# Optimization experiments

Hardware: AMD Instinct MI355X
Metric: run time of the kernel (lower is better)

The kernel has to match this reference:

```python
import jax, jax.numpy as jnp
import numpy as np

C, K, D, N = 8, 64, 32, 2048  # components, flow layers, obs dim, grid nodes


def setup_inputs() -> dict:
    key = jax.random.key(0)
    ks = jax.random.split(key, 16)
    def rn(k, shape, s=0.02):
        return (s * jax.random.normal(k, shape, dtype=jnp.float32))
    return {
        "nodes": jax.random.normal(ks[0], (N, D), dtype=jnp.float32),
        # coupling nets: MLP([D, 2D, D]) per layer per component (torch Linear layout: W [out,in])
        "s_W1": rn(ks[1], (C, K, 2 * D, D)), "s_b1": rn(ks[2], (C, K, 2 * D)),
        "s_W2": rn(ks[3], (C, K, D, 2 * D)), "s_b2": rn(ks[4], (C, K, D)),
        "t_W1": rn(ks[5], (C, K, 2 * D, D)), "t_b1": rn(ks[6], (C, K, 2 * D)),
        "t_W2": rn(ks[7], (C, K, D, 2 * D)), "t_b2": rn(ks[8], (C, K, D)),
        # ActNorm scale/shift per layer per component
        "an_s": rn(ks[9], (C, K, D), 0.01), "an_t": rn(ks[10], (C, K, D), 0.01),
        # DiagGaussian base distribution params per component
        "loc": rn(ks[11], (C, D), 0.1), "log_scale": rn(ks[12], (C, D), 0.1),
        # unconstrained joint S matrix
        "S_unc": rn(ks[13], (C, C), 0.5),
    }


def _mlp(x, W1, b1, W2, b2):
    # nf.nets.MLP default leaky=0.0 -> ReLU
    return jax.nn.relu(x @ W1.T + b1) @ W2.T + b2


def reference(nodes, s_W1, s_b1, s_W2, s_b2, t_W1, t_b1, t_W2, t_b2,
              an_s, an_t, loc, log_scale, S_unc):
    dt = nodes.dtype
    # alternating checkerboard masks: b=[1,0,1,0,...] for even layers, 1-b for odd
    b = (jnp.arange(D) % 2 == 0).astype(dt)
    masks = jnp.where((jnp.arange(K) % 2 == 0)[:, None], b, 1.0 - b)  # [K, D]

    def per_component(sW1, sb1, sW2, sb2, tW1, tb1, tW2, tb2, ans, ant, lc, ls):
        def step(carry, p):
            z, ld = carry
            w1s, b1s, w2s, b2s, w1t, b1t, w2t, b2t, a_s, a_t, m = p
            # ActNorm inverse: z = (z - t) * exp(-s); log_det -= sum(s)
            z = (z - a_t) * jnp.exp(-a_s)
            ld = ld - jnp.sum(a_s)
            # MaskedAffineFlow inverse
            zm = m * z
            s = _mlp(zm, w1s, b1s, w2s, b2s)
            t = _mlp(zm, w1t, b1t, w2t, b2t)
            z = zm + (1.0 - m) * (z - t) * jnp.exp(-s)
            ld = ld - jnp.sum((1.0 - m) * s, axis=-1)
            return (z, ld), None

        # log_prob applies flows in reverse order
        ps = tuple(a[::-1] for a in (sW1, sb1, sW2, sb2, tW1, tb1, tW2, tb2, ans, ant, masks))
        (z, ld), _ = jax.lax.scan(step, (nodes, jnp.zeros(nodes.shape[0], dt)), ps)
        # DiagGaussian log_prob
        logq = ld - 0.5 * D * jnp.log(2.0 * jnp.pi) \
               - jnp.sum(ls + 0.5 * ((z - lc) * jnp.exp(-ls)) ** 2, axis=-1)
        return logq  # [N]

    logp = jax.vmap(per_component)(s_W1, s_b1, s_W2, s_b2, t_W1, t_b1, t_W2, t_b2,
                                   an_s, an_t, loc, log_scale)  # [C, N]
    Bm = jnp.exp(logp)
    # torch F.normalize(p=1, dim=1): v / max(||v||_1, 1e-12)
    Bm = Bm / jnp.maximum(jnp.sum(jnp.abs(Bm), axis=1, keepdims=True), 1e-12)
    S = jnp.exp(S_unc)
    S = S / jnp.sum(S)
    return (Bm.T @ S @ Bm).astype(jnp.float32)  # [N, N]
```

## Files before the change

kernel.cpp:

```cpp
#include <hip/hip_runtime.h>
#include <math.h>
#include <stdint.h>

#define C_ 8
#define K_ 64
#define D_ 32
#define N_ 2048

typedef _Float16 f16x4 __attribute__((ext_vector_type(4)));
typedef float    f32x4 __attribute__((ext_vector_type(4)));

#define BLOBF 2304
#define BLOBB (BLOBF * 4)
#define OB1   2048
#define OB2   2176
#define OAN   2208


__device__ __forceinline__ f16x4 ldfrag(const char* p) {
  union { uint2 u; f16x4 h; } cv;
  cv.u = *(const uint2*)p;
  return cv.h;
}

__global__ __launch_bounds__(64) void k_pack(
    const float* __restrict__ sW1, const float* __restrict__ sb1,
    const float* __restrict__ sW2, const float* __restrict__ sb2,
    const float* __restrict__ tW1, const float* __restrict__ tb1,
    const float* __restrict__ tW2, const float* __restrict__ tb2,
    const float* __restrict__ an_s, const float* __restrict__ an_t,
    float* __restrict__ pk) {
  const int b = blockIdx.x;
  const int pin = b & 1;
  const int l = threadIdx.x;
  const int g = l >> 4, m15 = l & 15;
  float* dst = pk + (size_t)b * BLOBF;
  char* dstc = (char*)dst;

#pragma unroll
  for (int t = 0; t < 16; ++t) {
    const int mlp = t >> 3, tt = t & 7;
    const float* W1 = mlp ? tW1 : sW1;
    const float* W2 = mlp ? tW2 : sW2;
    union { uint2 u; f16x4 h; } cv;
    if (tt < 4) {
      const float* row = W1 + b * 2048 + (16 * tt + m15) * 32;
#pragma unroll
      for (int a = 0; a < 4; ++a) cv.h[a] = (_Float16)row[2 * (4 * g + a) + pin];
    } else {
      const float* row = W2 + b * 2048 + (2 * m15 + 1 - pin) * 64;
#pragma unroll
      for (int a = 0; a < 4; ++a) cv.h[a] = (_Float16)row[16 * (tt - 4) + 4 * g + a];
    }
    *(uint2*)(dstc + t * 512 + l * 8) = cv.u;
  }
#pragma unroll
  for (int i = l; i < 128; i += 64) {
    const int mlp = i >> 6, t = (i >> 4) & 3, gg = (i >> 2) & 3, r = i & 3;
    dst[OB1 + i] = (mlp ? tb1 : sb1)[b * 64 + 16 * t + 4 * gg + r];
  }
  if (l < 32) {
    const int mlp = l >> 4, gg = (l >> 2) & 3, r = l & 3;
    dst[OB2 + l] = (mlp ? tb2 : sb2)[b * 32 + 2 * (4 * gg + r) + 1 - pin];
  }
  {
    const int gg = l >> 4, slot = l & 15, j = slot & 3;
    const int par = slot >> 3, isEa = (slot >> 2) & 1;
    const int dim = 2 * (4 * gg + j) + par;
    dst[OAN + l] = isEa ? expf(-an_s[b * 32 + dim]) : an_t[b * 32 + dim];
  }
}

__global__ __launch_bounds__(512) void k_pre(const float* __restrict__ loc,
                                             const float* __restrict__ log_scale,
                                             float* __restrict__ ws) {
  const int i = threadIdx.x;
  const int c = i >> 6, gg = (i >> 4) & 3, slot = i & 15, j = slot & 3;
  const int par = slot >> 3, isE = (slot >> 2) & 1;
  const int dim = 2 * (4 * gg + j) + par;
  ws[i] = isE ? expf(-log_scale[c * 32 + dim]) : loc[c * 32 + dim];
}

__global__ __launch_bounds__(512) void k_const(const float* __restrict__ an_s,
                                               const float* __restrict__ log_scale,
                                               float* __restrict__ ws) {
  int tid = threadIdx.x;
  int c = tid >> 6, lane = tid & 63;
  float acc = 0.f;
  for (int r = 0; r < 32; ++r) acc += an_s[c * 2048 + r * 64 + lane];
  if (lane < 32) acc += log_scale[c * 32 + lane];
  for (int off = 32; off; off >>= 1) acc += __shfl_down(acc, off);
  if (lane == 0) ws[512 + c] = -acc - 29.406033062549525f;
}

template <int PIN>
__device__ __forceinline__ void layer_mfma(const char* bp, int g, int fo,
                                           float (&x)[4], float (&y)[4],
                                           float& ldp) {
  const float* bf = (const float*)bp;
  const f32x4 ane = *(const f32x4*)(bf + OAN + g * 16 + 0);
  const f32x4 aee = *(const f32x4*)(bf + OAN + g * 16 + 4);
  const f32x4 ano = *(const f32x4*)(bf + OAN + g * 16 + 8);
  const f32x4 aeo = *(const f32x4*)(bf + OAN + g * 16 + 12);
  const f32x4 atx = PIN ? ano : ane, eax = PIN ? aeo : aee;
  const f32x4 aty = PIN ? ane : ano, eay = PIN ? aee : aeo;
  f16x4 bx;
#pragma unroll
  for (int j = 0; j < 4; ++j) {
    x[j] = (x[j] - atx[j]) * eax[j];
    y[j] = (y[j] - aty[j]) * eay[j];
    bx[j] = (_Float16)x[j];
  }
  f32x4 c2s = *(const f32x4*)(bf + OB2 + g * 4);
  f32x4 c2t = *(const f32x4*)(bf + OB2 + 16 + g * 4);
#pragma unroll
  for (int t = 0; t < 4; ++t) {
    f32x4 c1 = *(const f32x4*)(bf + OB1 + (t * 4 + g) * 4);
    c1 = __builtin_amdgcn_mfma_f32_16x16x16f16(ldfrag(bp + t * 512 + fo), bx, c1, 0, 0, 0);
    f16x4 bh;
#pragma unroll
    for (int j = 0; j < 4; ++j) bh[j] = (_Float16)fmaxf(c1[j], 0.f);
    c2s = __builtin_amdgcn_mfma_f32_16x16x16f16(ldfrag(bp + (4 + t) * 512 + fo), bh, c2s, 0, 0, 0);
  }
#pragma unroll
  for (int t = 0; t < 4; ++t) {
    f32x4 c1 = *(const f32x4*)(bf + OB1 + 64 + (t * 4 + g) * 4);
    c1 = __builtin_amdgcn_mfma_f32_16x16x16f16(ldfrag(bp + (8 + t) * 512 + fo), bx, c1, 0, 0, 0);
    f16x4 bh;
#pragma unroll
    for (int j = 0; j < 4; ++j) bh[j] = (_Float16)fmaxf(c1[j], 0.f);
    c2t = __builtin_amdgcn_mfma_f32_16x16x16f16(ldfrag(bp + (12 + t) * 512 + fo), bh, c2t, 0, 0, 0);
  }
#pragma unroll
  for (int r = 0; r < 4; ++r) {
    const float sv = c2s[r];
    y[r] = (y[r] - c2t[r]) * __expf(-sv);
    ldp -= sv;
  }
}

__global__ __launch_bounds__(256) void k_flow(
    const float* __restrict__ nodes, const float* __restrict__ pk,
    const float* __restrict__ ws, float* __restrict__ logp) {
  const int l = threadIdx.x & 63;
  const int wv = threadIdx.x >> 6;
  const int g = l >> 4, m15 = l & 15;
  const int fo = l * 8;
  const int c = blockIdx.x & 7;
  const int nb = (blockIdx.x >> 3) * 64 + wv * 16;
  const int node = nb + m15;

  float xe[4], xo[4];
  {
    const float4 v0 = *(const float4*)(nodes + node * 32 + 8 * g);
    const float4 v1 = *(const float4*)(nodes + node * 32 + 8 * g + 4);
    xe[0] = v0.x; xo[0] = v0.y; xe[1] = v0.z; xo[1] = v0.w;
    xe[2] = v1.x; xo[2] = v1.y; xe[3] = v1.z; xo[3] = v1.w;
  }
  float ldp = 0.f;
  const char* bp0 = (const char*)pk + (size_t)(c * 64) * BLOBB;

#pragma unroll 1
  for (int k = 63; k > 0; k -= 2) {
    layer_mfma<1>(bp0 + (size_t)k * BLOBB, g, fo, xo, xe, ldp);
    layer_mfma<0>(bp0 + (size_t)(k - 1) * BLOBB, g, fo, xe, xo, ldp);
  }

  const float* lw = ws + (c * 4 + g) * 16;
  const f32x4 loce = *(const f32x4*)(lw + 0);
  const f32x4 else_ = *(const f32x4*)(lw + 4);
  const f32x4 loco = *(const f32x4*)(lw + 8);
  const f32x4 elso = *(const f32x4*)(lw + 12);
  float sq = 0.f;
#pragma unroll
  for (int j = 0; j < 4; ++j) {
    const float a = (xe[j] - loce[j]) * else_[j];
    const float b2v = (xo[j] - loco[j]) * elso[j];
    sq += a * a + b2v * b2v;
  }
  float part = ldp - 0.5f * sq;
  part += __shfl_xor(part, 16);
  part += __shfl_xor(part, 32);
  if (l < 16) logp[c * N_ + nb + l] = part + ws[512 + c];
}

__global__ __launch_bounds__(256) void k_norm(const float* __restrict__ logp,
                                              float* __restrict__ Bn) {
  __shared__ float red[256];
  const int c = blockIdx.x;
  const int t = threadIdx.x;
  float e[8];
  float part = 0.f;
#pragma unroll
  for (int r = 0; r < 8; ++r) {
    e[r] = __expf(logp[c * N_ + r * 256 + t]);
    part += e[r];
  }
  red[t] = part;
  __syncthreads();
  for (int s = 128; s > 0; s >>= 1) {
    if (t < s) red[t] += red[t + s];
    __syncthreads();
  }
  const float inv = 1.f / fmaxf(red[0], 1e-12f);
#pragma unroll
  for (int r = 0; r < 8; ++r) Bn[c * N_ + r * 256 + t] = e[r] * inv;
}

__global__ __launch_bounds__(256) void k_A(const float* __restrict__ S_unc,
                                           const float* __restrict__ Bn,
                                           float* __restrict__ A) {
  __shared__ float sE[64];
  __shared__ float sInv;
  const int t = threadIdx.x;
  if (t < 64) sE[t] = __expf(S_unc[t]);
  __syncthreads();
  if (t == 0) {
    float tot = 0.f;
    for (int i = 0; i < 64; ++i) tot += sE[i];
    sInv = 1.f / tot;
  }
  __syncthreads();
  const int j = blockIdx.x * 256 + t;
  float b[8];
#pragma unroll
  for (int cc = 0; cc < 8; ++cc) b[cc] = Bn[cc * N_ + j];
#pragma unroll
  for (int c = 0; c < 8; ++c) {
    float acc = 0.f;
#pragma unroll
    for (int cc = 0; cc < 8; ++cc) acc += sE[c * 8 + cc] * b[cc];
    A[c * N_ + j] = acc * sInv;
  }
}

__global__ __launch_bounds__(256) void k_out(const float* __restrict__ Bn,
                                             const float* __restrict__ A,
                                             float* __restrict__ out) {
  const int T = blockIdx.x * 256 + threadIdx.x;
  const int i0 = (T >> 9) << 2;
  const int j0 = (T & 511) << 2;
  float acc[4][4];
#pragma unroll
  for (int r = 0; r < 4; ++r)
#pragma unroll
    for (int e2 = 0; e2 < 4; ++e2) acc[r][e2] = 0.f;
#pragma unroll
  for (int cc = 0; cc < 8; ++cc) {
    const float4 bi = *(const float4*)(Bn + cc * N_ + i0);
    const float4 aj = *(const float4*)(A + cc * N_ + j0);
    const float br[4] = {bi.x, bi.y, bi.z, bi.w};
    const float ar[4] = {aj.x, aj.y, aj.z, aj.w};
#pragma unroll
    for (int r = 0; r < 4; ++r)
#pragma unroll
      for (int e2 = 0; e2 < 4; ++e2) acc[r][e2] += br[r] * ar[e2];
  }
#pragma unroll
  for (int r = 0; r < 4; ++r)
    *(float4*)(out + (i0 + r) * N_ + j0) =
        make_float4(acc[r][0], acc[r][1], acc[r][2], acc[r][3]);
}

extern "C" void kernel_launch(void* const* d_in, const int* in_sizes, int n_in,
                              void* d_out, int out_size, void* d_ws,
                              size_t ws_size, hipStream_t stream) {
  const float* nodes = (const float*)d_in[0];
  const float* sW1 = (const float*)d_in[1];
  const float* sb1 = (const float*)d_in[2];
  const float* sW2 = (const float*)d_in[3];
  const float* sb2 = (const float*)d_in[4];
  const float* tW1 = (const float*)d_in[5];
  const float* tb1 = (const float*)d_in[6];
  const float* tW2 = (const float*)d_in[7];
  const float* tb2 = (const float*)d_in[8];
  const float* an_s = (const float*)d_in[9];
  const float* an_t = (const float*)d_in[10];
  const float* loc = (const float*)d_in[11];
  const float* log_scale = (const float*)d_in[12];
  const float* S_unc = (const float*)d_in[13];
  float* out = (float*)d_out;
  float* ws = (float*)d_ws;

  float* pkw = out;
  float* logp = ws + 520;
  float* Bn = ws + 16904;
  float* A = ws + 33288;

  k_pack<<<512, 64, 0, stream>>>(sW1, sb1, sW2, sb2, tW1, tb1, tW2, tb2,
                                 an_s, an_t, pkw);
  k_pre<<<1, 512, 0, stream>>>(loc, log_scale, ws);
  k_const<<<1, 512, 0, stream>>>(an_s, log_scale, ws);

  k_flow<<<256, 256, 0, stream>>>(nodes, pkw, ws, logp);

  k_norm<<<8, 256, 0, stream>>>(logp, Bn);
  k_A<<<8, 256, 0, stream>>>(S_unc, Bn, A);
  k_out<<<1024, 256, 0, stream>>>(Bn, A, out);
}
```

Measured before the change: 197.3 us.

## Software-pipeline per-layer weight loads in flow kernel and merge prep kernels

The flow kernel now loads the next layer's packed weight fragments, biases and ActNorm params into registers (double-buffered LR structs) before computing the current layer, hiding global/L2 load latency behind MFMA work. The pack kernel uses 256 threads with vectorized float4 reads instead of scalar strided loads, and the two tiny setup kernels are merged into one launch. The register double buffer raises VGPR pressure, and launch_bounds(256,1) accepts lower occupancy.

```diff
diff --git a/kernel.cpp b/kernel.cpp
--- a/kernel.cpp
+++ b/kernel.cpp
@@ -17,13 +17,13 @@
 #define OAN   2208
 
 
-__device__ __forceinline__ f16x4 ldfrag(const char* p) {
+__device__ __forceinline__ f16x4 asf16(uint2 u) {
   union { uint2 u; f16x4 h; } cv;
-  cv.u = *(const uint2*)p;
+  cv.u = u;
   return cv.h;
 }
 
-__global__ __launch_bounds__(64) void k_pack(
+__global__ __launch_bounds__(256) void k_pack(
     const float* __restrict__ sW1, const float* __restrict__ sb1,
     const float* __restrict__ sW2, const float* __restrict__ sb2,
     const float* __restrict__ tW1, const float* __restrict__ tb1,
@@ -32,78 +32,106 @@
     float* __restrict__ pk) {
   const int b = blockIdx.x;
   const int pin = b & 1;
-  const int l = threadIdx.x;
+  const int tid = threadIdx.x;
+  const int wv = tid >> 6, l = tid & 63;
   const int g = l >> 4, m15 = l & 15;
   float* dst = pk + (size_t)b * BLOBF;
   char* dstc = (char*)dst;
 
 #pragma unroll
-  for (int t = 0; t < 16; ++t) {
+  for (int ti = 0; ti < 4; ++ti) {
+    const int t = wv * 4 + ti;
     const int mlp = t >> 3, tt = t & 7;
     const float* W1 = mlp ? tW1 : sW1;
     const float* W2 = mlp ? tW2 : sW2;
     union { uint2 u; f16x4 h; } cv;
     if (tt < 4) {
-      const float* row = W1 + b * 2048 + (16 * tt + m15) * 32;
-#pragma unroll
-      for (int a = 0; a < 4; ++a) cv.h[a] = (_Float16)row[2 * (4 * g + a) + pin];
+      const float* row = W1 + b * 2048 + (16 * tt + m15) * 32 + 8 * g;
+      const float4 u0 = *(const float4*)(row);
+      const float4 u1 = *(const float4*)(row + 4);
+      if (pin == 0) {
+        cv.h[0] = (_Float16)u0.x; cv.h[1] = (_Float16)u0.z;
+        cv.h[2] = (_Float16)u1.x; cv.h[3] = (_Float16)u1.z;
+      } else {
+        cv.h[0] = (_Float16)u0.y; cv.h[1] = (_Float16)u0.w;
+        cv.h[2] = (_Float16)u1.y; cv.h[3] = (_Float16)u1.w;
+      }
     } else {
-      const float* row = W2 + b * 2048 + (2 * m15 + 1 - pin) * 64;
-#pragma unroll
-      for (int a = 0; a < 4; ++a) cv.h[a] = (_Float16)row[16 * (tt - 4) + 4 * g + a];
+      const float* row = W2 + b * 2048 + (2 * m15 + 1 - pin) * 64 + 16 * (tt - 4) + 4 * g;
+      const float4 v = *(const float4*)row;
+      cv.h[0] = (_Float16)v.x; cv.h[1] = (_Float16)v.y;
+      cv.h[2] = (_Float16)v.z; cv.h[3] = (_Float16)v.w;
     }
     *(uint2*)(dstc + t * 512 + l * 8) = cv.u;
   }
-#pragma unroll
-  for (int i = l; i < 128; i += 64) {
+  if (tid < 128) {
+    const int i = tid;
     const int mlp = i >> 6, t = (i >> 4) & 3, gg = (i >> 2) & 3, r = i & 3;
     dst[OB1 + i] = (mlp ? tb1 : sb1)[b * 64 + 16 * t + 4 * gg + r];
-  }
-  if (l < 32) {
-    const int mlp = l >> 4, gg = (l >> 2) & 3, r = l & 3;
-    dst[OB2 + l] = (mlp ? tb2 : sb2)[b * 32 + 2 * (4 * gg + r) + 1 - pin];
-  }
-  {
-    const int gg = l >> 4, slot = l & 15, j = slot & 3;
+  } else if (tid < 160) {
+    const int i = tid - 128;
+    const int mlp = i >> 4, gg = (i >> 2) & 3, r = i & 3;
+    dst[OB2 + i] = (mlp ? tb2 : sb2)[b * 32 + 2 * (4 * gg + r) + 1 - pin];
+  } else if (tid < 224) {
+    const int i = tid - 160;
+    const int gg = i >> 4, slot = i & 15, j = slot & 3;
     const int par = slot >> 3, isEa = (slot >> 2) & 1;
     const int dim = 2 * (4 * gg + j) + par;
-    dst[OAN + l] = isEa ? expf(-an_s[b * 32 + dim]) : an_t[b * 32 + dim];
-  }
-}
-
-__global__ __launch_bounds__(512) void k_pre(const float* __restrict__ loc,
-                                             const float* __restrict__ log_scale,
-                                             float* __restrict__ ws) {
+    dst[OAN + i] = isEa ? expf(-an_s[b * 32 + dim]) : an_t[b * 32 + dim];
+  }
+}
+
+__global__ __launch_bounds__(512) void k_misc(const float* __restrict__ loc,
+                                              const float* __restrict__ log_scale,
+                                              const float* __restrict__ an_s,
+                                              float* __restrict__ ws) {
   const int i = threadIdx.x;
-  const int c = i >> 6, gg = (i >> 4) & 3, slot = i & 15, j = slot & 3;
-  const int par = slot >> 3, isE = (slot >> 2) & 1;
-  const int dim = 2 * (4 * gg + j) + par;
-  ws[i] = isE ? expf(-log_scale[c * 32 + dim]) : loc[c * 32 + dim];
-}
-
-__global__ __launch_bounds__(512) void k_const(const float* __restrict__ an_s,
-                                               const float* __restrict__ log_scale,
-                                               float* __restrict__ ws) {
-  int tid = threadIdx.x;
-  int c = tid >> 6, lane = tid & 63;
-  float acc = 0.f;
-  for (int r = 0; r < 32; ++r) acc += an_s[c * 2048 + r * 64 + lane];
-  if (lane < 32) acc += log_scale[c * 32 + lane];
-  for (int off = 32; off; off >>= 1) acc += __shfl_down(acc, off);
-  if (lane == 0) ws[512 + c] = -acc - 29.406033062549525f;
+  {
+    const int c = i >> 6, gg = (i >> 4) & 3, slot = i & 15, j = slot & 3;
+    const int par = slot >> 3, isE = (slot >> 2) & 1;
+    const int dim = 2 * (4 * gg + j) + par;
+    ws[i] = isE ? expf(-log_scale[c * 32 + dim]) : loc[c * 32 + dim];
+  }
+  {
+    const int c = i >> 6, lane = i & 63;
+    float acc = 0.f;
+    for (int r = 0; r < 32; ++r) acc += an_s[c * 2048 + r * 64 + lane];
+    if (lane < 32) acc += log_scale[c * 32 + lane];
+    for (int off = 32; off; off >>= 1) acc += __shfl_down(acc, off);
+    if (lane == 0) ws[512 + c] = -acc - 29.406033062549525f;
+  }
+}
+
+struct LR {
+  uint2 fr[16];
+  f32x4 b1s[4], b1t[4];
+  f32x4 b2s, b2t;
+  f32x4 ane, aee, ano, aeo;
+};
+
+__device__ __forceinline__ void load_layer(const char* __restrict__ bp, int g,
+                                           int fo, LR& R) {
+#pragma unroll
+  for (int t = 0; t < 16; ++t) R.fr[t] = *(const uint2*)(bp + t * 512 + fo);
+  const float* bf = (const float*)bp;
+#pragma unroll
+  for (int t = 0; t < 4; ++t) {
+    R.b1s[t] = *(const f32x4*)(bf + OB1 + (t * 4 + g) * 4);
+    R.b1t[t] = *(const f32x4*)(bf + OB1 + 64 + (t * 4 + g) * 4);
+  }
+  R.b2s = *(const f32x4*)(bf + OB2 + g * 4);
+  R.b2t = *(const f32x4*)(bf + OB2 + 16 + g * 4);
+  R.ane = *(const f32x4*)(bf + OAN + g * 16 + 0);
+  R.aee = *(const f32x4*)(bf + OAN + g * 16 + 4);
+  R.ano = *(const f32x4*)(bf + OAN + g * 16 + 8);
+  R.aeo = *(const f32x4*)(bf + OAN + g * 16 + 12);
 }
 
 template <int PIN>
-__device__ __forceinline__ void layer_mfma(const char* bp, int g, int fo,
-                                           float (&x)[4], float (&y)[4],
-                                           float& ldp) {
-  const float* bf = (const float*)bp;
-  const f32x4 ane = *(const f32x4*)(bf + OAN + g * 16 + 0);
-  const f32x4 aee = *(const f32x4*)(bf + OAN + g * 16 + 4);
-  const f32x4 ano = *(const f32x4*)(bf + OAN + g * 16 + 8);
-  const f32x4 aeo = *(const f32x4*)(bf + OAN + g * 16 + 12);
-  const f32x4 atx = PIN ? ano : ane, eax = PIN ? aeo : aee;
-  const f32x4 aty = PIN ? ane : ano, eay = PIN ? aee : aeo;
+__device__ __forceinline__ void layer_mfma(const LR& R, float (&x)[4],
+                                           float (&y)[4], float& ldp) {
+  const f32x4 atx = PIN ? R.ano : R.ane, eax = PIN ? R.aeo : R.aee;
+  const f32x4 aty = PIN ? R.ane : R.ano, eay = PIN ? R.aee : R.aeo;
   f16x4 bx;
 #pragma unroll
   for (int j = 0; j < 4; ++j) {
@@ -111,25 +139,24 @@
     y[j] = (y[j] - aty[j]) * eay[j];
     bx[j] = (_Float16)x[j];
   }
-  f32x4 c2s = *(const f32x4*)(bf + OB2 + g * 4);
-  f32x4 c2t = *(const f32x4*)(bf + OB2 + 16 + g * 4);
+  f32x4 c2s = R.b2s, c2t = R.b2t;
 #pragma unroll
   for (int t = 0; t < 4; ++t) {
-    f32x4 c1 = *(const f32x4*)(bf + OB1 + (t * 4 + g) * 4);
-    c1 = __builtin_amdgcn_mfma_f32_16x16x16f16(ldfrag(bp + t * 512 + fo), bx, c1, 0, 0, 0);
+    f32x4 c1 = R.b1s[t];
+    c1 = __builtin_amdgcn_mfma_f32_16x16x16f16(asf16(R.fr[t]), bx, c1, 0, 0, 0);
     f16x4 bh;
 #pragma unroll
     for (int j = 0; j < 4; ++j) bh[j] = (_Float16)fmaxf(c1[j], 0.f);
-    c2s = __builtin_amdgcn_mfma_f32_16x16x16f16(ldfrag(bp + (4 + t) * 512 + fo), bh, c2s, 0, 0, 0);
+    c2s = __builtin_amdgcn_mfma_f32_16x16x16f16(asf16(R.fr[4 + t]), bh, c2s, 0, 0, 0);
   }
 #pragma unroll
   for (int t = 0; t < 4; ++t) {
-    f32x4 c1 = *(const f32x4*)(bf + OB1 + 64 + (t * 4 + g) * 4);
-    c1 = __builtin_amdgcn_mfma_f32_16x16x16f16(ldfrag(bp + (8 + t) * 512 + fo), bx, c1, 0, 0, 0);
+    f32x4 c1 = R.b1t[t];
+    c1 = __builtin_amdgcn_mfma_f32_16x16x16f16(asf16(R.fr[8 + t]), bx, c1, 0, 0, 0);
     f16x4 bh;
 #pragma unroll
     for (int j = 0; j < 4; ++j) bh[j] = (_Float16)fmaxf(c1[j], 0.f);
-    c2t = __builtin_amdgcn_mfma_f32_16x16x16f16(ldfrag(bp + (12 + t) * 512 + fo), bh, c2t, 0, 0, 0);
+    c2t = __builtin_amdgcn_mfma_f32_16x16x16f16(asf16(R.fr[12 + t]), bh, c2t, 0, 0, 0);
   }
 #pragma unroll
   for (int r = 0; r < 4; ++r) {
@@ -139,7 +166,7 @@
   }
 }
 
-__global__ __launch_bounds__(256) void k_flow(
+__global__ __launch_bounds__(256, 1) void k_flow(
     const float* __restrict__ nodes, const float* __restrict__ pk,
     const float* __restrict__ ws, float* __restrict__ logp) {
   const int l = threadIdx.x & 63;
@@ -160,10 +187,15 @@
   float ldp = 0.f;
   const char* bp0 = (const char*)pk + (size_t)(c * 64) * BLOBB;
 
+  LR RA, RB;
+  load_layer(bp0 + (size_t)63 * BLOBB, g, fo, RA);
+
 #pragma unroll 1
   for (int k = 63; k > 0; k -= 2) {
-    layer_mfma<1>(bp0 + (size_t)k * BLOBB, g, fo, xo, xe, ldp);
-    layer_mfma<0>(bp0 + (size_t)(k - 1) * BLOBB, g, fo, xe, xo, ldp);
+    load_layer(bp0 + (size_t)(k - 1) * BLOBB, g, fo, RB);
+    layer_mfma<1>(RA, xo, xe, ldp);
+    if (k > 1) load_layer(bp0 + (size_t)(k - 2) * BLOBB, g, fo, RA);
+    layer_mfma<0>(RB, xe, xo, ldp);
   }
 
   const float* lw = ws + (c * 4 + g) * 16;
@@ -287,10 +319,9 @@
   float* Bn = ws + 16904;
   float* A = ws + 33288;
 
-  k_pack<<<512, 64, 0, stream>>>(sW1, sb1, sW2, sb2, tW1, tb1, tW2, tb2,
-                                 an_s, an_t, pkw);
-  k_pre<<<1, 512, 0, stream>>>(loc, log_scale, ws);
-  k_const<<<1, 512, 0, stream>>>(an_s, log_scale, ws);
+  k_pack<<<512, 256, 0, stream>>>(sW1, sb1, sW2, sb2, tW1, tb1, tW2, tb2,
+                                  an_s, an_t, pkw);
+  k_misc<<<1, 512, 0, stream>>>(loc, log_scale, an_s, ws);
 
   k_flow<<<256, 256, 0, stream>>>(nodes, pkw, ws, logp);
 
```

New measurement: 187.3 us. -5.1%, faster.
